# Kernel optimization log

Hardware: AMD Instinct MI355X
Metric: run time of the kernel (lower is better)

## Reference

```python
import jax, jax.numpy as jnp
import numpy as np

N_CLS = 20
EMBED_DIM = 256


def setup_inputs() -> dict:
    key = jax.random.key(0)
    k1, k2 = jax.random.split(key)
    patch_embed = jax.random.normal(k1, (64, 4096, EMBED_DIM), dtype=jnp.float32)
    # xavier_uniform init for codebook: bound = sqrt(6/(fan_in+fan_out))
    bound = float(np.sqrt(6.0 / (N_CLS + EMBED_DIM)))
    codebook = jax.random.uniform(k2, (N_CLS, EMBED_DIM), dtype=jnp.float32,
                                  minval=-bound, maxval=bound)
    return {"patch_embed": patch_embed, "codebook": codebook}


def reference(patch_embed, codebook):
    # scores: (B, n_cls, N) = codebook (c,d) . patch_embed (b,n,d)
    attn = jnp.einsum('cd,bnd->bcn', codebook, patch_embed)
    attn = jax.nn.softmax(attn, axis=-1)
    # attn_patch: (B, n_cls, D)
    return jnp.einsum('bcn,bnd->bcd', attn, patch_embed)
```

## Files before the change

### kernel.cpp

```cpp
#include <hip/hip_runtime.h>
#include <cmath>

#define BATCH 64
#define NTOK  4096
#define DIM   256
#define NCLS  20
#define TILE  32
#define XPAD  65

#define GLOAD_LDS16(gp, lp) \
  __builtin_amdgcn_global_load_lds((const __attribute__((address_space(1))) void*)(gp), \
                                   (__attribute__((address_space(3))) void*)(lp), 16, 0, 0)

__device__ __forceinline__ float wave_sum64(float v) {
  #pragma unroll
  for (int m = 32; m >= 1; m >>= 1) v += __shfl_xor(v, m, 64);
  return v;
}

__global__ __launch_bounds__(256, 2) void patch_attn_chunk(
    const float* __restrict__ patch, const float* __restrict__ codebook,
    float* __restrict__ o_ws, float* __restrict__ l_ws, int nch) {
  __shared__ float4 Xs[TILE * XPAD];
  __shared__ float4 CBs[NCLS * (DIM / 4)];
  __shared__ float4 Ps4[4 * TILE];
  __shared__ float  Ps1[4 * TILE];

  const int tid  = threadIdx.x;
  const int w    = tid >> 6;
  const int lane = tid & 63;
  const int r    = lane & 31;
  const int h    = lane >> 5;
  const int b    = blockIdx.x / nch;
  const int ch   = blockIdx.x - b * nch;
  const int rows = NTOK / nch;
  const int ntiles = rows / TILE;
  const float4* Xg  = (const float4*)patch + ((size_t)b * NTOK + (size_t)ch * rows) * (DIM / 4);
  const float4* cb4 = (const float4*)codebook;
  const int c0 = __builtin_amdgcn_readfirstlane(w * 5);

  #pragma unroll
  for (int i = 0; i < 5; ++i)
    GLOAD_LDS16(cb4 + i * 256 + w * 64 + lane, &CBs[i * 256 + w * 64 + lane]);

  float4 o[5];
  float l_run[5];
  #pragma unroll
  for (int j = 0; j < 5; ++j) {
    o[j] = make_float4(0.f, 0.f, 0.f, 0.f);
    l_run[j] = 0.f;
  }

  for (int t = 0; t < ntiles; ++t) {
    const float4* srcT = Xg + (size_t)t * TILE * (DIM / 4);
    #pragma unroll
    for (int i = 0; i < 8; ++i) {
      const int n = i * 4 + w;
      GLOAD_LDS16(srcT + n * (DIM / 4) + lane, &Xs[n * XPAD + lane]);
    }
    __syncthreads();

    float s[5] = {0.f, 0.f, 0.f, 0.f, 0.f};
    {
      const int xb  = r * XPAD + h * 32;
      const int cbb = h * 32;
      #pragma unroll 8
      for (int cbi = 0; cbi < 32; ++cbi) {
        float4 x = Xs[xb + cbi];
        #pragma unroll
        for (int j = 0; j < 5; ++j) {
          float4 cv = CBs[(c0 + j) * (DIM / 4) + cbb + cbi];
          s[j] = fmaf(x.x, cv.x, s[j]);
          s[j] = fmaf(x.y, cv.y, s[j]);
          s[j] = fmaf(x.z, cv.z, s[j]);
          s[j] = fmaf(x.w, cv.w, s[j]);
        }
      }
    }
    float p[5];
    #pragma unroll
    for (int j = 0; j < 5; ++j) {
      s[j] += __shfl_xor(s[j], 32, 64);
      p[j] = __expf(s[j]);
      l_run[j] += p[j];
    }

    Ps4[w * TILE + r] = make_float4(p[0], p[1], p[2], p[3]);
    Ps1[w * TILE + r] = p[4];

    #pragma unroll 8
    for (int n = 0; n < TILE; ++n) {
      float4 x  = Xs[n * XPAD + lane];
      float4 pv = Ps4[w * TILE + n];
      float  p4 = Ps1[w * TILE + n];
      o[0].x = fmaf(pv.x, x.x, o[0].x); o[0].y = fmaf(pv.x, x.y, o[0].y);
      o[0].z = fmaf(pv.x, x.z, o[0].z); o[0].w = fmaf(pv.x, x.w, o[0].w);
      o[1].x = fmaf(pv.y, x.x, o[1].x); o[1].y = fmaf(pv.y, x.y, o[1].y);
      o[1].z = fmaf(pv.y, x.z, o[1].z); o[1].w = fmaf(pv.y, x.w, o[1].w);
      o[2].x = fmaf(pv.z, x.x, o[2].x); o[2].y = fmaf(pv.z, x.y, o[2].y);
      o[2].z = fmaf(pv.z, x.z, o[2].z); o[2].w = fmaf(pv.z, x.w, o[2].w);
      o[3].x = fmaf(pv.w, x.x, o[3].x); o[3].y = fmaf(pv.w, x.y, o[3].y);
      o[3].z = fmaf(pv.w, x.z, o[3].z); o[3].w = fmaf(pv.w, x.w, o[3].w);
      o[4].x = fmaf(p4,   x.x, o[4].x); o[4].y = fmaf(p4,   x.y, o[4].y);
      o[4].z = fmaf(p4,   x.z, o[4].z); o[4].w = fmaf(p4,   x.w, o[4].w);
    }
    __syncthreads();
  }

  const size_t base = (size_t)(b * nch + ch) * NCLS + c0;
  float4* og = (float4*)o_ws;
  #pragma unroll
  for (int j = 0; j < 5; ++j) og[(base + j) * (DIM / 4) + lane] = o[j];
  #pragma unroll
  for (int j = 0; j < 5; ++j) l_run[j] = 0.5f * wave_sum64(l_run[j]);
  if (lane == 0) {
    #pragma unroll
    for (int j = 0; j < 5; ++j) l_ws[base + j] = l_run[j];
  }
}

__global__ __launch_bounds__(256) void patch_attn_combine(
    const float* __restrict__ o_ws, const float* __restrict__ l_ws,
    float* __restrict__ out, int nch) {
  const int bc = blockIdx.x;
  const int b = bc / NCLS;
  const int c = bc - b * NCLS;
  const int d = threadIdx.x;

  float lg = 0.f, acc = 0.f;
  for (int ch = 0; ch < nch; ++ch) {
    size_t idx = ((size_t)b * nch + ch) * NCLS + c;
    lg  += l_ws[idx];
    acc += o_ws[idx * DIM + d];
  }
  out[(size_t)bc * DIM + d] = acc / lg;
}

extern "C" void kernel_launch(void* const* d_in, const int* in_sizes, int n_in,
                              void* d_out, int out_size, void* d_ws, size_t ws_size,
                              hipStream_t stream) {
  const float* patch = (const float*)d_in[0];
  const float* cbk   = (const float*)d_in[1];
  float* out = (float*)d_out;

  int nch = 8;
  while (nch > 1 && (size_t)BATCH * nch * NCLS * (DIM + 1) * sizeof(float) > ws_size) nch >>= 1;

  float* o_ws = (float*)d_ws;
  float* l_ws = o_ws + (size_t)BATCH * nch * NCLS * DIM;

  patch_attn_chunk<<<dim3(BATCH * nch), dim3(256), 0, stream>>>(patch, cbk, o_ws, l_ws, nch);
  patch_attn_combine<<<dim3(BATCH * NCLS), dim3(256), 0, stream>>>(o_ws, l_ws, out, nch);
}
```

Before: 410.8 us.

## Fuse score and accumulation per row with register codebook and DPP reductions

Keeps each wave's slice of the codebook in registers, pre-scaled by log2(e) so exp2f can be used. Each half-wave processes one token row at a time, reducing dot products with DPP row ops plus one shuffle, and accumulates p*x directly into registers. This removes the shared-memory probability buffers and the codebook LDS reads. It also raises the launch-bound occupancy hint and doubles the token chunk count for more blocks. The cost is a cross-lane reduction and exp per row per class, heavier register use, and duplicated exp work across lanes.

```diff
diff --git a/kernel.cpp b/kernel.cpp
--- a/kernel.cpp
+++ b/kernel.cpp
@@ -12,25 +12,36 @@
   __builtin_amdgcn_global_load_lds((const __attribute__((address_space(1))) void*)(gp), \
                                    (__attribute__((address_space(3))) void*)(lp), 16, 0, 0)
 
+template <int CTRL>
+__device__ __forceinline__ float dpp_add(float v) {
+  int x = __builtin_amdgcn_update_dpp(0, __float_as_int(v), CTRL, 0xF, 0xF, false);
+  return v + __int_as_float(x);
+}
+
+__device__ __forceinline__ float allreduce32(float v) {
+  v = dpp_add<0x128>(v);
+  v = dpp_add<0x124>(v);
+  v = dpp_add<0x122>(v);
+  v = dpp_add<0x121>(v);
+  return v + __shfl_xor(v, 16, 64);
+}
+
 __device__ __forceinline__ float wave_sum64(float v) {
   #pragma unroll
   for (int m = 32; m >= 1; m >>= 1) v += __shfl_xor(v, m, 64);
   return v;
 }
 
-__global__ __launch_bounds__(256, 2) void patch_attn_chunk(
+__global__ __launch_bounds__(256, 4) void patch_attn_chunk(
     const float* __restrict__ patch, const float* __restrict__ codebook,
     float* __restrict__ o_ws, float* __restrict__ l_ws, int nch) {
   __shared__ float4 Xs[TILE * XPAD];
-  __shared__ float4 CBs[NCLS * (DIM / 4)];
-  __shared__ float4 Ps4[4 * TILE];
-  __shared__ float  Ps1[4 * TILE];
 
   const int tid  = threadIdx.x;
   const int w    = tid >> 6;
   const int lane = tid & 63;
-  const int r    = lane & 31;
-  const int h    = lane >> 5;
+  const int r    = lane >> 5;
+  const int s    = lane & 31;
   const int b    = blockIdx.x / nch;
   const int ch   = blockIdx.x - b * nch;
   const int rows = NTOK / nch;
@@ -39,15 +50,23 @@
   const float4* cb4 = (const float4*)codebook;
   const int c0 = __builtin_amdgcn_readfirstlane(w * 5);
 
+  float4 cb[5][2];
   #pragma unroll
-  for (int i = 0; i < 5; ++i)
-    GLOAD_LDS16(cb4 + i * 256 + w * 64 + lane, &CBs[i * 256 + w * 64 + lane]);
+  for (int j = 0; j < 5; ++j) {
+    #pragma unroll
+    for (int i = 0; i < 2; ++i) {
+      float4 v = cb4[(c0 + j) * (DIM / 4) + 2 * s + i];
+      const float k = 1.4426950408889634f;
+      cb[j][i] = make_float4(v.x * k, v.y * k, v.z * k, v.w * k);
+    }
+  }
 
-  float4 o[5];
+  float4 o[5][2];
   float l_run[5];
   #pragma unroll
   for (int j = 0; j < 5; ++j) {
-    o[j] = make_float4(0.f, 0.f, 0.f, 0.f);
+    o[j][0] = make_float4(0.f, 0.f, 0.f, 0.f);
+    o[j][1] = make_float4(0.f, 0.f, 0.f, 0.f);
     l_run[j] = 0.f;
   }
 
@@ -60,59 +79,58 @@
     }
     __syncthreads();
 
-    float s[5] = {0.f, 0.f, 0.f, 0.f, 0.f};
-    {
-      const int xb  = r * XPAD + h * 32;
-      const int cbb = h * 32;
-      #pragma unroll 8
-      for (int cbi = 0; cbi < 32; ++cbi) {
-        float4 x = Xs[xb + cbi];
-        #pragma unroll
-        for (int j = 0; j < 5; ++j) {
-          float4 cv = CBs[(c0 + j) * (DIM / 4) + cbb + cbi];
-          s[j] = fmaf(x.x, cv.x, s[j]);
-          s[j] = fmaf(x.y, cv.y, s[j]);
-          s[j] = fmaf(x.z, cv.z, s[j]);
-          s[j] = fmaf(x.w, cv.w, s[j]);
-        }
+    #pragma unroll 4
+    for (int g = 0; g < 16; ++g) {
+      const int R = 2 * g + r;
+      float4 x0 = Xs[R * XPAD + 2 * s];
+      float4 x1 = Xs[R * XPAD + 2 * s + 1];
+      #pragma unroll
+      for (int j = 0; j < 5; ++j) {
+        float sj = x0.x * cb[j][0].x;
+        sj = fmaf(x0.y, cb[j][0].y, sj);
+        sj = fmaf(x0.z, cb[j][0].z, sj);
+        sj = fmaf(x0.w, cb[j][0].w, sj);
+        sj = fmaf(x1.x, cb[j][1].x, sj);
+        sj = fmaf(x1.y, cb[j][1].y, sj);
+        sj = fmaf(x1.z, cb[j][1].z, sj);
+        sj = fmaf(x1.w, cb[j][1].w, sj);
+        sj = allreduce32(sj);
+        float p = exp2f(sj);
+        l_run[j] += p;
+        o[j][0].x = fmaf(p, x0.x, o[j][0].x);
+        o[j][0].y = fmaf(p, x0.y, o[j][0].y);
+        o[j][0].z = fmaf(p, x0.z, o[j][0].z);
+        o[j][0].w = fmaf(p, x0.w, o[j][0].w);
+        o[j][1].x = fmaf(p, x1.x, o[j][1].x);
+        o[j][1].y = fmaf(p, x1.y, o[j][1].y);
+        o[j][1].z = fmaf(p, x1.z, o[j][1].z);
+        o[j][1].w = fmaf(p, x1.w, o[j][1].w);
       }
-    }
-    float p[5];
-    #pragma unroll
-    for (int j = 0; j < 5; ++j) {
-      s[j] += __shfl_xor(s[j], 32, 64);
-      p[j] = __expf(s[j]);
-      l_run[j] += p[j];
-    }
-
-    Ps4[w * TILE + r] = make_float4(p[0], p[1], p[2], p[3]);
-    Ps1[w * TILE + r] = p[4];
-
-    #pragma unroll 8
-    for (int n = 0; n < TILE; ++n) {
-      float4 x  = Xs[n * XPAD + lane];
-      float4 pv = Ps4[w * TILE + n];
-      float  p4 = Ps1[w * TILE + n];
-      o[0].x = fmaf(pv.x, x.x, o[0].x); o[0].y = fmaf(pv.x, x.y, o[0].y);
-      o[0].z = fmaf(pv.x, x.z, o[0].z); o[0].w = fmaf(pv.x, x.w, o[0].w);
-      o[1].x = fmaf(pv.y, x.x, o[1].x); o[1].y = fmaf(pv.y, x.y, o[1].y);
-      o[1].z = fmaf(pv.y, x.z, o[1].z); o[1].w = fmaf(pv.y, x.w, o[1].w);
-      o[2].x = fmaf(pv.z, x.x, o[2].x); o[2].y = fmaf(pv.z, x.y, o[2].y);
-      o[2].z = fmaf(pv.z, x.z, o[2].z); o[2].w = fmaf(pv.z, x.w, o[2].w);
-      o[3].x = fmaf(pv.w, x.x, o[3].x); o[3].y = fmaf(pv.w, x.y, o[3].y);
-      o[3].z = fmaf(pv.w, x.z, o[3].z); o[3].w = fmaf(pv.w, x.w, o[3].w);
-      o[4].x = fmaf(p4,   x.x, o[4].x); o[4].y = fmaf(p4,   x.y, o[4].y);
-      o[4].z = fmaf(p4,   x.z, o[4].z); o[4].w = fmaf(p4,   x.w, o[4].w);
     }
     __syncthreads();
   }
 
+  #pragma unroll
+  for (int j = 0; j < 5; ++j) {
+    #pragma unroll
+    for (int i = 0; i < 2; ++i) {
+      o[j][i].x += __shfl_xor(o[j][i].x, 32, 64);
+      o[j][i].y += __shfl_xor(o[j][i].y, 32, 64);
+      o[j][i].z += __shfl_xor(o[j][i].z, 32, 64);
+      o[j][i].w += __shfl_xor(o[j][i].w, 32, 64);
+    }
+    l_run[j] = wave_sum64(l_run[j]) * (1.0f / 32.0f);
+  }
+
   const size_t base = (size_t)(b * nch + ch) * NCLS + c0;
   float4* og = (float4*)o_ws;
-  #pragma unroll
-  for (int j = 0; j < 5; ++j) og[(base + j) * (DIM / 4) + lane] = o[j];
-  #pragma unroll
-  for (int j = 0; j < 5; ++j) l_run[j] = 0.5f * wave_sum64(l_run[j]);
+  if (r == 0) {
+    #pragma unroll
+    for (int j = 0; j < 5; ++j) {
+      og[(base + j) * (DIM / 4) + 2 * s    ] = o[j][0];
+      og[(base + j) * (DIM / 4) + 2 * s + 1] = o[j][1];
+    }
+  }
   if (lane == 0) {
     #pragma unroll
     for (int j = 0; j < 5; ++j) l_ws[base + j] = l_run[j];
@@ -143,7 +161,7 @@
   const float* cbk   = (const float*)d_in[1];
   float* out = (float*)d_out;
 
-  int nch = 8;
+  int nch = 16;
   while (nch > 1 && (size_t)BATCH * nch * NCLS * (DIM + 1) * sizeof(float) > ws_size) nch >>= 1;
 
   float* o_ws = (float*)d_ws;
```

Result: slower. 424.1 us (+3.2%).
